# Performance work log

Measured on AMD Instinct MI355X. Metric: run time of the kernel, lower is better.

Reference implementation:

```python
import jax, jax.numpy as jnp
import numpy as np
import math

R1 = 1.0
R2 = 4.0
NBINS_XY = 4
NBINS_ZY = 4
PARTITIONS = NBINS_XY * NBINS_ZY * 2  # 32
TOPK = 200
TWO_PI = 2.0 * math.pi
PI = math.pi


def setup_inputs() -> dict:
    key = jax.random.key(0)
    k1, k2 = jax.random.split(key)
    # LiDAR-like coordinates, ~[-30, 30] meters
    sampled_vehicle_points = jax.random.normal(k1, (1024, 3), dtype=jnp.float32) * 20.0
    fusion_point = jax.random.normal(k2, (20000, 3), dtype=jnp.float32) * 20.0
    return {"sampled_vehicle_points": sampled_vehicle_points, "fusion_point": fusion_point}


def _compute_partitions_batch(q):
    # q: [S, K, 3]. rel[b, i, j] = q[b, j] - q[b, i]  (A.unsqueeze(1) - B.unsqueeze(2))
    rel = q[:, None, :, :] - q[:, :, None, :]  # [S, K, K, 3]
    angles_xy = jnp.fmod(jnp.arctan2(rel[..., 1], rel[..., 0]) + TWO_PI, TWO_PI)
    angles_zy = jnp.fmod(jnp.arctan2(rel[..., 1], rel[..., 2]) + TWO_PI, PI)
    xy_bins = jnp.floor(angles_xy / (TWO_PI / NBINS_XY))
    zy_bins = jnp.floor(angles_zy / (PI / NBINS_ZY))
    # hash(A, B, seed=NBINS_ZY): -1 where either < 0
    angle_ok = (xy_bins >= 0) & (zy_bins >= 0)
    angles_bins = jnp.where(angle_ok, xy_bins * NBINS_ZY + zy_bins, -1.0)
    D = jnp.sqrt(jnp.sum(rel * rel, axis=-1) + 1e-7)  # [S, K, K]
    dist_bins = jnp.where(D >= R2, 1.0, jnp.where(D >= R1, 0.0, -1.0))
    bin_ok = (dist_bins >= 0) & (angles_bins >= 0)
    bins = jnp.where(bin_ok, dist_bins * (NBINS_XY * NBINS_ZY) + angles_bins, -1.0)
    return bins  # [S, K, K] float, -1 for ignored


def reference(sampled_vehicle_points, fusion_point):
    # kNN query: K nearest fusion points for each sampled vehicle point
    d2 = jnp.sum(
        (sampled_vehicle_points[:, None, :] - fusion_point[None, :, :]) ** 2, axis=-1
    )  # [S, Nf]
    _, idx = jax.lax.top_k(-d2, TOPK)  # indices of TOPK smallest distances
    queried = fusion_point[idx]  # [S, K, 3]

    bins = _compute_partitions_batch(queried)  # [S, K, K]
    row0 = bins[:, 0, :]  # [S, K] — only row 0 is used by the loss
    # points_in_partition[s, p] = sum_j (row0[s, j] == p) + 1
    counts = jnp.sum(
        row0[:, :, None] == jnp.arange(PARTITIONS, dtype=bins.dtype)[None, None, :],
        axis=1,
    ).astype(jnp.float32) + 1.0  # [S, P]
    pip = counts / jnp.linalg.norm(counts, axis=-1, keepdims=True) * 4.0
    gt_dist = jax.nn.softmax(pip, axis=-1)
    return gt_dist
```

## Files before the change

kernel.cpp:

```cpp
#include <hip/hip_runtime.h>
#include <math.h>

#define KTOP 200
#define NPART 32
#define BLOCK 512
#define NHIST 2048
#define CAND_CAP 2048
#define TLIST_CAP 1024
#define WCAP 256
#define SSTAR 28

__device__ __forceinline__ float d2_ref(float ax, float ay, float az,
                                        float bx, float by, float bz) {
    float dx = __fsub_rn(ax, bx), dy = __fsub_rn(ay, by), dz = __fsub_rn(az, bz);
    return __fadd_rn(__fadd_rn(__fmul_rn(dx, dx), __fmul_rn(dy, dy)), __fmul_rn(dz, dz));
}

__device__ __forceinline__ unsigned key_of(const float* __restrict__ fus, int j,
                                           float vx, float vy, float vz) {
    return __float_as_uint(d2_ref(vx, vy, vz, fus[3*j], fus[3*j+1], fus[3*j+2]));
}

__device__ __forceinline__ int compute_bin(float rx, float ry, float rz) {
    const float TWO_PI_F = (float)6.283185307179586;
    const float PI_F     = (float)3.141592653589793;
    const float XY_W     = (float)(6.283185307179586 / 4.0);
    const float ZY_W     = (float)(3.141592653589793 / 4.0);

    float d2 = __fadd_rn(__fadd_rn(__fmul_rn(rx, rx), __fmul_rn(ry, ry)), __fmul_rn(rz, rz));
    float D  = sqrtf(__fadd_rn(d2, 1e-7f));
    float dist_bin;
    if (D >= 4.0f)      dist_bin = 1.0f;
    else if (D >= 1.0f) dist_bin = 0.0f;
    else                return -1;

    float axy = fmodf(atan2f(ry, rx) + TWO_PI_F, TWO_PI_F);
    float azy = fmodf(atan2f(ry, rz) + TWO_PI_F, PI_F);
    float xyb = floorf(__fdiv_rn(axy, XY_W));
    float zyb = floorf(__fdiv_rn(azy, ZY_W));
    if (!(xyb >= 0.0f && zyb >= 0.0f)) return -1;
    float ab  = xyb * 4.0f + zyb;
    int bin = (int)(dist_bin * 16.0f + ab);
    return bin;
}

__global__ __launch_bounds__(BLOCK, 8)
void shape_context_kernel(const float* __restrict__ veh,
                          const float* __restrict__ fus,
                          float* __restrict__ out,
                          int nfus) {
    const int b   = blockIdx.x;
    const int tid = threadIdx.x;
    const int lane = tid & 63;
    const int wid  = tid >> 6;

    __shared__ unsigned int hist[NHIST];
    __shared__ unsigned long long cand[CAND_CAP];
    __shared__ unsigned long long tlist[TLIST_CAP];
    __shared__ int wlist[WCAP];
    __shared__ unsigned int hist32[NPART];
    __shared__ unsigned int waveTot[BLOCK / 64];
    __shared__ unsigned int waveBase[BLOCK / 64];
    __shared__ unsigned int s_bucket, s_rem, s_bcount;
    __shared__ int s_candCount, s_wcount, s_tcount;
    __shared__ unsigned long long s_minPacked, s_serMin, s_lowBound;

    const float vx = veh[b * 3 + 0], vy = veh[b * 3 + 1], vz = veh[b * 3 + 2];
    const float4* fus4 = (const float4*)fus;
    const int ntrip = nfus >> 2;

    if (tid == 0) { s_minPacked = ~0ull; s_candCount = 0; s_wcount = 0; s_tcount = 0; }
    for (int i = tid; i < NHIST; i += BLOCK) hist[i] = 0;
    if (tid < NPART) hist32[tid] = 0;
    __syncthreads();

    auto find_bucket = [&](unsigned remq) {
        const int PER = NHIST / BLOCK;
        int base = tid * PER;
        unsigned c[PER];
        unsigned p = 0;
        #pragma unroll
        for (int i = 0; i < PER; i++) { c[i] = hist[base + i]; p += c[i]; }
        unsigned incl = p;
        #pragma unroll
        for (int d = 1; d < 64; d <<= 1) {
            unsigned n = __shfl_up(incl, d, 64);
            if (lane >= d) incl += n;
        }
        if (lane == 63) waveTot[wid] = incl;
        __syncthreads();
        if (tid == 0) {
            unsigned acc = 0;
            for (int w = 0; w < BLOCK / 64; w++) { waveBase[w] = acc; acc += waveTot[w]; }
        }
        __syncthreads();
        unsigned excl = waveBase[wid] + incl - p;
        if (excl < remq && remq <= excl + p) {
            unsigned cum = excl;
            #pragma unroll
            for (int i = 0; i < PER; i++) {
                if (cum + c[i] >= remq) { s_bucket = base + i; s_rem = remq - cum; s_bcount = c[i]; break; }
                cum += c[i];
            }
        }
        __syncthreads();
    };

    {
        int j = (int)(((long long)tid * nfus) / BLOCK);
        unsigned k = key_of(fus, j, vx, vy, vz);
        atomicAdd(&hist[k >> 21], 1u);
    }
    __syncthreads();
    find_bucket(SSTAR);
    const unsigned Pb = s_bucket + 1;
    __syncthreads();

    for (int m = tid; m < ntrip; m += BLOCK) {
        float4 A = fus4[3 * m], Bq = fus4[3 * m + 1], Cq = fus4[3 * m + 2];
        unsigned k0 = __float_as_uint(d2_ref(vx, vy, vz, A.x,  A.y,  A.z));
        unsigned k1 = __float_as_uint(d2_ref(vx, vy, vz, A.w,  Bq.x, Bq.y));
        unsigned k2 = __float_as_uint(d2_ref(vx, vy, vz, Bq.z, Bq.w, Cq.x));
        unsigned k3 = __float_as_uint(d2_ref(vx, vy, vz, Cq.y, Cq.z, Cq.w));
        int jb = 4 * m;
        if ((k0 >> 21) < Pb) { int pos = atomicAdd(&s_candCount, 1); if (pos < CAND_CAP) cand[pos] = ((unsigned long long)k0 << 32) | (unsigned)(jb + 0); }
        if ((k1 >> 21) < Pb) { int pos = atomicAdd(&s_candCount, 1); if (pos < CAND_CAP) cand[pos] = ((unsigned long long)k1 << 32) | (unsigned)(jb + 1); }
        if ((k2 >> 21) < Pb) { int pos = atomicAdd(&s_candCount, 1); if (pos < CAND_CAP) cand[pos] = ((unsigned long long)k2 << 32) | (unsigned)(jb + 2); }
        if ((k3 >> 21) < Pb) { int pos = atomicAdd(&s_candCount, 1); if (pos < CAND_CAP) cand[pos] = ((unsigned long long)k3 << 32) | (unsigned)(jb + 3); }
    }
    for (int j = (nfus & ~3) + tid; j < nfus; j += BLOCK) {
        unsigned k = key_of(fus, j, vx, vy, vz);
        if ((k >> 21) < Pb) { int pos = atomicAdd(&s_candCount, 1); if (pos < CAND_CAP) cand[pos] = ((unsigned long long)k << 32) | (unsigned)j; }
    }
    __syncthreads();

    const int cnt = s_candCount;
    unsigned rem;

    if (cnt >= KTOP && cnt <= CAND_CAP) {
        unsigned long long lm = ~0ull;
        for (int i = tid; i < cnt; i += BLOCK) lm = min(lm, cand[i]);
        #pragma unroll
        for (int d = 32; d > 0; d >>= 1) {
            unsigned long long o = __shfl_xor(lm, d, 64);
            lm = (o < lm) ? o : lm;
        }
        if (lane == 0) atomicMin(&s_minPacked, lm);

        for (int i = tid; i < NHIST; i += BLOCK) hist[i] = 0;
        __syncthreads();
        for (int i = tid; i < cnt; i += BLOCK) atomicAdd(&hist[(unsigned)(cand[i] >> 53)], 1u);
        __syncthreads();
        find_bucket(KTOP);
        const unsigned T2 = s_bucket;
        rem = s_rem;
        const unsigned bcount = s_bcount;

        if (bcount <= TLIST_CAP) {
            for (int i = tid; i < cnt; i += BLOCK) {
                unsigned bk = (unsigned)(cand[i] >> 53);
                if (bk < T2) {
                    int pos = atomicAdd(&s_wcount, 1);
                    if (pos < WCAP) wlist[pos] = (int)(cand[i] & 0xFFFFFFFFull);
                } else if (bk == T2) {
                    int pos = atomicAdd(&s_tcount, 1);
                    if (pos < TLIST_CAP) tlist[pos] = cand[i];
                }
            }
            __syncthreads();
            const int tc = s_tcount;
            for (int i = tid; i < tc; i += BLOCK) {
                unsigned long long me = tlist[i];
                int rank = 0;
                for (int k2 = 0; k2 < tc; k2++) rank += (tlist[k2] < me) ? 1 : 0;
                if (rank < (int)rem) {
                    int pos = atomicAdd(&s_wcount, 1);
                    if (pos < WCAP) wlist[pos] = (int)(me & 0xFFFFFFFFull);
                }
            }
        } else {
            for (int i = tid; i < cnt; i += BLOCK) {
                unsigned bk = (unsigned)(cand[i] >> 53);
                if (bk < T2) {
                    int pos = atomicAdd(&s_wcount, 1);
                    if (pos < WCAP) wlist[pos] = (int)(cand[i] & 0xFFFFFFFFull);
                }
            }
            __syncthreads();
            for (int i = tid; i < cnt; i += BLOCK) {
                unsigned long long me = cand[i];
                if ((unsigned)(me >> 53) == T2) {
                    int rank = 0;
                    for (int k2 = 0; k2 < cnt; k2++) {
                        unsigned long long o = cand[k2];
                        rank += ((unsigned)(o >> 53) == T2 && o < me) ? 1 : 0;
                    }
                    if (rank < (int)rem) {
                        int pos = atomicAdd(&s_wcount, 1);
                        if (pos < WCAP) wlist[pos] = (int)(me & 0xFFFFFFFFull);
                    }
                }
            }
        }
        __syncthreads();
    } else {
        if (tid == 0) s_candCount = 0;
        for (int i = tid; i < NHIST; i += BLOCK) hist[i] = 0;
        __syncthreads();
        for (int j = tid; j < nfus; j += BLOCK)
            atomicAdd(&hist[key_of(fus, j, vx, vy, vz) >> 21], 1u);
        __syncthreads();
        find_bucket(KTOP);
        unsigned T = s_bucket;
        rem = s_rem;
        unsigned bcount = s_bcount;
        int shift = 21;

        while (bcount > CAND_CAP && shift > 0) {
            int newshift = (shift > 11) ? (shift - 11) : 0;
            unsigned digmask = (1u << (shift - newshift)) - 1;
            __syncthreads();
            for (int i = tid; i < NHIST; i += BLOCK) hist[i] = 0;
            __syncthreads();
            for (int j = tid; j < nfus; j += BLOCK) {
                unsigned k = key_of(fus, j, vx, vy, vz);
                if ((k >> shift) == T) atomicAdd(&hist[(k >> newshift) & digmask], 1u);
            }
            __syncthreads();
            find_bucket(rem);
            T = (T << (shift - newshift)) | s_bucket;
            rem = s_rem;
            bcount = s_bcount;
            shift = newshift;
        }

        for (int j = tid; j < nfus; j += BLOCK) {
            unsigned k = key_of(fus, j, vx, vy, vz);
            unsigned hi = k >> shift;
            if (hi < T) {
                int pos = atomicAdd(&s_wcount, 1);
                if (pos < WCAP) wlist[pos] = j;
                atomicMin(&s_minPacked, ((unsigned long long)k << 32) | (unsigned)j);
            } else if (hi == T) {
                int pos = atomicAdd(&s_candCount, 1);
                if (pos < CAND_CAP) cand[pos] = ((unsigned long long)k << 32) | (unsigned)j;
                atomicMin(&s_minPacked, ((unsigned long long)k << 32) | (unsigned)j);
            }
        }
        __syncthreads();
        const int fcnt = s_candCount;
        if (fcnt <= CAND_CAP) {
            for (int i = tid; i < fcnt; i += BLOCK) {
                unsigned long long me = cand[i];
                int rank = 0;
                for (int k2 = 0; k2 < fcnt; k2++) rank += (cand[k2] < me) ? 1 : 0;
                if (rank < (int)rem) {
                    int pos = atomicAdd(&s_wcount, 1);
                    if (pos < WCAP) wlist[pos] = (int)(me & 0xFFFFFFFFull);
                }
            }
            __syncthreads();
        } else {
            const int idx0f = (int)(s_minPacked & 0xFFFFFFFFull);
            const float fq0x = fus[idx0f * 3], fq0y = fus[idx0f * 3 + 1], fq0z = fus[idx0f * 3 + 2];
            if (tid == 0) s_lowBound = 0;
            __syncthreads();
            for (unsigned itx = 0; itx < rem; ++itx) {
                if (tid == 0) s_serMin = ~0ull;
                __syncthreads();
                unsigned long long lowB = s_lowBound;
                unsigned long long lmx = ~0ull;
                for (int j = tid; j < nfus; j += BLOCK) {
                    unsigned k = key_of(fus, j, vx, vy, vz);
                    if ((k >> shift) == T) {
                        unsigned long long p = ((unsigned long long)k << 32) | (unsigned)j;
                        if (p >= lowB && p < lmx) lmx = p;
                    }
                }
                #pragma unroll
                for (int d = 32; d > 0; d >>= 1) {
                    unsigned long long o = __shfl_xor(lmx, d, 64);
                    lmx = (o < lmx) ? o : lmx;
                }
                if (lane == 0) atomicMin(&s_serMin, lmx);
                __syncthreads();
                if (tid == 0) {
                    int jm = (int)(s_serMin & 0xFFFFFFFFull);
                    float fx = fus[jm * 3], fy = fus[jm * 3 + 1], fz = fus[jm * 3 + 2];
                    int bin = compute_bin(__fsub_rn(fx, fq0x), __fsub_rn(fy, fq0y), __fsub_rn(fz, fq0z));
                    if (bin >= 0 && bin < NPART) hist32[bin] += 1u;
                    s_lowBound = s_serMin + 1;
                }
                __syncthreads();
            }
        }
    }

    const int idx0 = (int)(s_minPacked & 0xFFFFFFFFull);
    const float q0x = fus[idx0 * 3], q0y = fus[idx0 * 3 + 1], q0z = fus[idx0 * 3 + 2];
    {
        int wc = s_wcount; if (wc > WCAP) wc = WCAP;
        for (int i = tid; i < wc; i += BLOCK) {
            int j = wlist[i];
            float fx = fus[3 * j], fy = fus[3 * j + 1], fz = fus[3 * j + 2];
            int bin = compute_bin(__fsub_rn(fx, q0x), __fsub_rn(fy, q0y), __fsub_rn(fz, q0z));
            if (bin >= 0 && bin < NPART) atomicAdd(&hist32[bin], 1u);
        }
    }
    __syncthreads();

    if (tid < NPART) {
        float c = (float)hist32[tid] + 1.0f;
        float ss = __fmul_rn(c, c);
        #pragma unroll
        for (int d = 16; d > 0; d >>= 1) ss += __shfl_xor(ss, d, 64);
        float v = __fmul_rn(__fdiv_rn(c, sqrtf(ss)), 4.0f);
        float mx = v;
        #pragma unroll
        for (int d = 16; d > 0; d >>= 1) mx = fmaxf(mx, __shfl_xor(mx, d, 64));
        float e = expf(v - mx);
        float sum = e;
        #pragma unroll
        for (int d = 16; d > 0; d >>= 1) sum += __shfl_xor(sum, d, 64);
        out[b * NPART + tid] = __fdiv_rn(e, sum);
    }
}

extern "C" void kernel_launch(void* const* d_in, const int* in_sizes, int n_in,
                              void* d_out, int out_size, void* d_ws, size_t ws_size,
                              hipStream_t stream) {
    const float* veh = (const float*)d_in[0];
    const float* fus = (const float*)d_in[1];
    float* out = (float*)d_out;
    int nveh = in_sizes[0] / 3;
    int nfus = in_sizes[1] / 3;
    shape_context_kernel<<<nveh, BLOCK, 0, stream>>>(veh, fus, out, nfus);
}
```

Before: 89.98 us.

## Stage fusion points through shared-memory tiles and retry candidate threshold adaptively

The candidate scan now copies fusion points into a shared-memory tile with coalesced float4 loads, then computes distances from shared memory. The tile aliases the histogram buffer. The sampling threshold uses a smaller quantile and an exact bucket rather than bucket+1. If the candidate count falls outside [KTOP, CAND_CAP], the bucket is nudged and the scan repeated up to a limit before falling back to radix select. The smaller candidate cap and the removal of tlist cut LDS use, which may allow more resident blocks. The cost is extra block barriers per tile and possible full rescans when a retry is needed.

```diff
diff --git a/kernel.cpp b/kernel.cpp
--- a/kernel.cpp
+++ b/kernel.cpp
@@ -5,10 +5,12 @@
 #define NPART 32
 #define BLOCK 512
 #define NHIST 2048
-#define CAND_CAP 2048
-#define TLIST_CAP 1024
+#define CAND_CAP 1200
 #define WCAP 256
-#define SSTAR 28
+#define SSTAR 20
+#define TS 2048
+#define TSF4 (TS * 3 / 4)
+#define MAX_RETRY 8
 
 __device__ __forceinline__ float d2_ref(float ax, float ay, float az,
                                         float bx, float by, float bz) {
@@ -54,25 +56,22 @@
     const int lane = tid & 63;
     const int wid  = tid >> 6;
 
-    __shared__ unsigned int hist[NHIST];
+    __shared__ __align__(16) char smem[TSF4 * 16];
+    float4*   tile4 = (float4*)smem;
+    unsigned* hist  = (unsigned*)smem;
+
     __shared__ unsigned long long cand[CAND_CAP];
-    __shared__ unsigned long long tlist[TLIST_CAP];
     __shared__ int wlist[WCAP];
-    __shared__ unsigned int hist32[NPART];
-    __shared__ unsigned int waveTot[BLOCK / 64];
-    __shared__ unsigned int waveBase[BLOCK / 64];
-    __shared__ unsigned int s_bucket, s_rem, s_bcount;
-    __shared__ int s_candCount, s_wcount, s_tcount;
+    __shared__ unsigned hist32[NPART];
+    __shared__ unsigned waveTot[BLOCK / 64], waveBase[BLOCK / 64];
+    __shared__ unsigned s_bucket, s_rem, s_bcount;
+    __shared__ int s_candCount, s_wcount;
     __shared__ unsigned long long s_minPacked, s_serMin, s_lowBound;
 
-    const float vx = veh[b * 3 + 0], vy = veh[b * 3 + 1], vz = veh[b * 3 + 2];
-    const float4* fus4 = (const float4*)fus;
-    const int ntrip = nfus >> 2;
-
-    if (tid == 0) { s_minPacked = ~0ull; s_candCount = 0; s_wcount = 0; s_tcount = 0; }
-    for (int i = tid; i < NHIST; i += BLOCK) hist[i] = 0;
+    const float vx = veh[3*b], vy = veh[3*b+1], vz = veh[3*b+2];
+
+    if (tid == 0) { s_minPacked = ~0ull; s_wcount = 0; }
     if (tid < NPART) hist32[tid] = 0;
-    __syncthreads();
 
     auto find_bucket = [&](unsigned remq) {
         const int PER = NHIST / BLOCK;
@@ -106,38 +105,60 @@
         __syncthreads();
     };
 
+    for (int i = tid; i < NHIST; i += BLOCK) hist[i] = 0;
+    __syncthreads();
     {
         int j = (int)(((long long)tid * nfus) / BLOCK);
-        unsigned k = key_of(fus, j, vx, vy, vz);
-        atomicAdd(&hist[k >> 21], 1u);
+        atomicAdd(&hist[key_of(fus, j, vx, vy, vz) >> 21], 1u);
     }
     __syncthreads();
     find_bucket(SSTAR);
-    const unsigned Pb = s_bucket + 1;
-    __syncthreads();
-
-    for (int m = tid; m < ntrip; m += BLOCK) {
-        float4 A = fus4[3 * m], Bq = fus4[3 * m + 1], Cq = fus4[3 * m + 2];
-        unsigned k0 = __float_as_uint(d2_ref(vx, vy, vz, A.x,  A.y,  A.z));
-        unsigned k1 = __float_as_uint(d2_ref(vx, vy, vz, A.w,  Bq.x, Bq.y));
-        unsigned k2 = __float_as_uint(d2_ref(vx, vy, vz, Bq.z, Bq.w, Cq.x));
-        unsigned k3 = __float_as_uint(d2_ref(vx, vy, vz, Cq.y, Cq.z, Cq.w));
-        int jb = 4 * m;
-        if ((k0 >> 21) < Pb) { int pos = atomicAdd(&s_candCount, 1); if (pos < CAND_CAP) cand[pos] = ((unsigned long long)k0 << 32) | (unsigned)(jb + 0); }
-        if ((k1 >> 21) < Pb) { int pos = atomicAdd(&s_candCount, 1); if (pos < CAND_CAP) cand[pos] = ((unsigned long long)k1 << 32) | (unsigned)(jb + 1); }
-        if ((k2 >> 21) < Pb) { int pos = atomicAdd(&s_candCount, 1); if (pos < CAND_CAP) cand[pos] = ((unsigned long long)k2 << 32) | (unsigned)(jb + 2); }
-        if ((k3 >> 21) < Pb) { int pos = atomicAdd(&s_candCount, 1); if (pos < CAND_CAP) cand[pos] = ((unsigned long long)k3 << 32) | (unsigned)(jb + 3); }
-    }
-    for (int j = (nfus & ~3) + tid; j < nfus; j += BLOCK) {
-        unsigned k = key_of(fus, j, vx, vy, vz);
-        if ((k >> 21) < Pb) { int pos = atomicAdd(&s_candCount, 1); if (pos < CAND_CAP) cand[pos] = ((unsigned long long)k << 32) | (unsigned)j; }
-    }
-    __syncthreads();
-
-    const int cnt = s_candCount;
-    unsigned rem;
-
-    if (cnt >= KTOP && cnt <= CAND_CAP) {
+    unsigned Pb = s_bucket;
+    if (Pb == 0) Pb = 1;
+
+    const int nq4 = nfus & ~3;
+    int cnt = 0, attempts = 0;
+    bool needRadix = false;
+    while (true) {
+        if (tid == 0) s_candCount = 0;
+        for (int base = 0; base < nq4; base += TS) {
+            int npts = min(TS, nq4 - base);
+            int nf4  = (npts * 3) >> 2;
+            const float4* g4 = (const float4*)fus + ((base * 3) >> 2);
+            __syncthreads();
+            for (int i = tid; i < nf4; i += BLOCK) tile4[i] = g4[i];
+            __syncthreads();
+            int quads = npts >> 2;
+            if (tid < quads) {
+                float4 A  = tile4[3 * tid];
+                float4 Bq = tile4[3 * tid + 1];
+                float4 Cq = tile4[3 * tid + 2];
+                unsigned k0 = __float_as_uint(d2_ref(vx, vy, vz, A.x,  A.y,  A.z));
+                unsigned k1 = __float_as_uint(d2_ref(vx, vy, vz, A.w,  Bq.x, Bq.y));
+                unsigned k2 = __float_as_uint(d2_ref(vx, vy, vz, Bq.z, Bq.w, Cq.x));
+                unsigned k3 = __float_as_uint(d2_ref(vx, vy, vz, Cq.y, Cq.z, Cq.w));
+                int jb = base + 4 * tid;
+                if ((k0 >> 21) < Pb) { int pos = atomicAdd(&s_candCount, 1); if (pos < CAND_CAP) cand[pos] = ((unsigned long long)k0 << 32) | (unsigned)(jb + 0); }
+                if ((k1 >> 21) < Pb) { int pos = atomicAdd(&s_candCount, 1); if (pos < CAND_CAP) cand[pos] = ((unsigned long long)k1 << 32) | (unsigned)(jb + 1); }
+                if ((k2 >> 21) < Pb) { int pos = atomicAdd(&s_candCount, 1); if (pos < CAND_CAP) cand[pos] = ((unsigned long long)k2 << 32) | (unsigned)(jb + 2); }
+                if ((k3 >> 21) < Pb) { int pos = atomicAdd(&s_candCount, 1); if (pos < CAND_CAP) cand[pos] = ((unsigned long long)k3 << 32) | (unsigned)(jb + 3); }
+            }
+        }
+        for (int j = nq4 + tid; j < nfus; j += BLOCK) {
+            unsigned k = key_of(fus, j, vx, vy, vz);
+            if ((k >> 21) < Pb) { int pos = atomicAdd(&s_candCount, 1); if (pos < CAND_CAP) cand[pos] = ((unsigned long long)k << 32) | (unsigned)j; }
+        }
+        __syncthreads();
+        cnt = s_candCount;
+        if (cnt >= KTOP && cnt <= CAND_CAP) break;
+        if (++attempts >= MAX_RETRY) { needRadix = true; break; }
+        if (cnt < KTOP) Pb += 1;
+        else { if (Pb <= 1) { needRadix = true; break; } Pb -= 1; }
+    }
+
+    unsigned rem = 0;
+
+    if (!needRadix) {
         unsigned long long lm = ~0ull;
         for (int i = tid; i < cnt; i += BLOCK) lm = min(lm, cand[i]);
         #pragma unroll
@@ -154,57 +175,31 @@
         find_bucket(KTOP);
         const unsigned T2 = s_bucket;
         rem = s_rem;
-        const unsigned bcount = s_bcount;
-
-        if (bcount <= TLIST_CAP) {
-            for (int i = tid; i < cnt; i += BLOCK) {
-                unsigned bk = (unsigned)(cand[i] >> 53);
-                if (bk < T2) {
-                    int pos = atomicAdd(&s_wcount, 1);
-                    if (pos < WCAP) wlist[pos] = (int)(cand[i] & 0xFFFFFFFFull);
-                } else if (bk == T2) {
-                    int pos = atomicAdd(&s_tcount, 1);
-                    if (pos < TLIST_CAP) tlist[pos] = cand[i];
-                }
-            }
-            __syncthreads();
-            const int tc = s_tcount;
-            for (int i = tid; i < tc; i += BLOCK) {
-                unsigned long long me = tlist[i];
+
+        for (int i = tid; i < cnt; i += BLOCK) {
+            unsigned long long me = cand[i];
+            if ((unsigned)(me >> 53) < T2) {
+                int pos = atomicAdd(&s_wcount, 1);
+                if (pos < WCAP) wlist[pos] = (int)(me & 0xFFFFFFFFull);
+            }
+        }
+        for (int i = tid; i < cnt; i += BLOCK) {
+            unsigned long long me = cand[i];
+            if ((unsigned)(me >> 53) == T2) {
                 int rank = 0;
-                for (int k2 = 0; k2 < tc; k2++) rank += (tlist[k2] < me) ? 1 : 0;
+                for (int k2 = 0; k2 < cnt; k2++) {
+                    unsigned long long o = cand[k2];
+                    rank += ((unsigned)(o >> 53) == T2 && o < me) ? 1 : 0;
+                }
                 if (rank < (int)rem) {
                     int pos = atomicAdd(&s_wcount, 1);
                     if (pos < WCAP) wlist[pos] = (int)(me & 0xFFFFFFFFull);
                 }
             }
-        } else {
-            for (int i = tid; i < cnt; i += BLOCK) {
-                unsigned bk = (unsigned)(cand[i] >> 53);
-                if (bk < T2) {
-                    int pos = atomicAdd(&s_wcount, 1);
-                    if (pos < WCAP) wlist[pos] = (int)(cand[i] & 0xFFFFFFFFull);
-                }
-            }
-            __syncthreads();
-            for (int i = tid; i < cnt; i += BLOCK) {
-                unsigned long long me = cand[i];
-                if ((unsigned)(me >> 53) == T2) {
-                    int rank = 0;
-                    for (int k2 = 0; k2 < cnt; k2++) {
-                        unsigned long long o = cand[k2];
-                        rank += ((unsigned)(o >> 53) == T2 && o < me) ? 1 : 0;
-                    }
-                    if (rank < (int)rem) {
-                        int pos = atomicAdd(&s_wcount, 1);
-                        if (pos < WCAP) wlist[pos] = (int)(me & 0xFFFFFFFFull);
-                    }
-                }
-            }
         }
         __syncthreads();
     } else {
-        if (tid == 0) s_candCount = 0;
+        if (tid == 0) { s_candCount = 0; s_wcount = 0; }
         for (int i = tid; i < NHIST; i += BLOCK) hist[i] = 0;
         __syncthreads();
         for (int j = tid; j < nfus; j += BLOCK)
```

Result: slower. 194.6 us (+116.3%).
